# Kernel optimization log

Hardware: AMD Instinct MI355X
Metric: run time of the kernel (lower is better)

The kernel has to match this reference:

```python
import jax, jax.numpy as jnp
import numpy as np

E = 8        # n_experts
K = 2        # n_activated_experts (top_k)
D = 1024     # dim
B, N = 4, 4096
DC = 512     # dim_cond


def setup_inputs() -> dict:
    key = jax.random.key(0)
    ks = jax.random.split(key, 6)
    x = jax.random.normal(ks[0], (B, N, D), jnp.float32)
    cond = jax.random.normal(ks[1], (B, N, DC), jnp.float32)
    mask = jnp.ones((B, N), jnp.float32)
    W_shared = jax.random.normal(ks[2], (D, D), jnp.float32) * 0.02
    W_expert = jax.random.normal(ks[3], (D, D), jnp.float32) * 0.02
    W_gate = jax.random.normal(ks[4], (D, E - 1), jnp.float32) * 0.02
    bias = jnp.zeros((D,), jnp.float32)
    return dict(x=x, cond=cond, mask=mask, W_shared=W_shared,
                W_expert=W_expert, W_gate=W_gate, bias=bias)


def reference(x, cond, mask, W_shared, W_expert, W_gate, bias):
    b, n, d = x.shape
    T = b * n
    xf = x.reshape(T, d)

    # ---- router: softmax gate over E-1 logits, top-k, normalize ----
    scores = jax.nn.softmax(xf @ W_gate, axis=-1)            # [T, E-1]
    expert_weights, _ = jax.lax.top_k(scores, K)             # [T, K]
    expert_weights = expert_weights / expert_weights.sum(-1, keepdims=True)
    # uniform_expert_assignment=True: indices are arange % E
    expert_indices = (jnp.arange(T * K) % E).reshape(T, K)

    te = expert_indices.reshape(-1)                          # [T*K] flat assignments
    w = expert_weights.reshape(-1)                           # [T*K]

    capacity = (K * T) // E                                  # expert_capacity

    # ---- indices_and_bins: stable sort by expert, histogram, cumsum ----
    order = jnp.argsort(te, stable=True)                     # permutation into sorted order
    sorted_e = te[order]
    hist = jnp.bincount(te, length=E)                        # tokens_per_expert
    starts = jnp.concatenate([jnp.zeros((1,), hist.dtype), jnp.cumsum(hist)[:-1]])
    pos = jnp.arange(T * K) - starts[sorted_e]               # rank within expert bin
    valid = pos < capacity                                   # capacity drop
    dest = jnp.where(valid, sorted_e * capacity + pos, E * capacity)
    tok = order // K                                         # source token index

    # ---- binned_gather: [E*capacity, d] buffer, overflow row dropped ----
    gathered = jnp.zeros((E * capacity + 1, d), x.dtype).at[dest].set(xf[tok])
    gathered = gathered[:-1]

    # ---- expert compute on binned tokens ----
    y = gathered @ W_expert.T                                # [E*capacity, d]

    # ---- binned_scatter: weighted combine back to tokens ----
    contrib = w[order][:, None] * y[jnp.minimum(dest, E * capacity - 1)]
    moe_out = jnp.zeros((T, d), x.dtype).at[tok].add(
        jnp.where(valid[:, None], contrib, 0.0))

    shared = xf @ W_shared.T                                 # shared expert
    out = (shared + moe_out + bias).reshape(b, n, d)
    return out
```

## Files before the change

### kernel.cpp

```cpp
#include <hip/hip_runtime.h>
#include <hip/hip_bf16.h>
#include <stdint.h>

static constexpr int Mdim = 16384;
static constexpr int Ndim = 1024;
static constexpr int Kdim = 1024;
static constexpr int BM = 128, BN = 128, BK = 64;

typedef __attribute__((ext_vector_type(8))) __bf16 bf16x8;
typedef __attribute__((ext_vector_type(4))) float f32x4;
typedef __attribute__((ext_vector_type(8))) unsigned short ushort8;

__device__ inline unsigned short f2bf_rn(float f) {
    union { float f; uint32_t u; } v; v.f = f;
    uint32_t u = v.u;
    uint32_t r = u + 0x7FFFu + ((u >> 16) & 1u);
    return (unsigned short)(r >> 16);
}

__device__ inline uint32_t pack_bf2(float a, float b) {
    union { float f; uint32_t u; } ua, ub;
    ua.f = a; ub.f = b;
    uint32_t x = ua.u + 0x8000u;
    uint32_t y = ub.u + 0x8000u;
    return (x >> 16) | (y & 0xFFFF0000u);
}

__global__ __launch_bounds__(256) void cvt_w_kernel(const float* __restrict__ ws,
                                                    const float* __restrict__ we,
                                                    unsigned short* __restrict__ wc) {
    const size_t i = ((size_t)blockIdx.x * 256 + threadIdx.x) * 8;
    const f32x4* p0 = (const f32x4*)(ws + i);
    const f32x4* p1 = (const f32x4*)(we + i);
    f32x4 a0 = p0[0], a1 = p0[1], b0 = p1[0], b1 = p1[1];
    ushort8 o;
    o[0] = f2bf_rn(a0[0] + b0[0]); o[1] = f2bf_rn(a0[1] + b0[1]);
    o[2] = f2bf_rn(a0[2] + b0[2]); o[3] = f2bf_rn(a0[3] + b0[3]);
    o[4] = f2bf_rn(a1[0] + b1[0]); o[5] = f2bf_rn(a1[1] + b1[1]);
    o[6] = f2bf_rn(a1[2] + b1[2]); o[7] = f2bf_rn(a1[3] + b1[3]);
    *(ushort8*)(wc + i) = o;
}

__device__ inline void gload16(const void* g, void* l) {
    __builtin_amdgcn_global_load_lds((const __attribute__((address_space(1))) void*)g,
                                     (__attribute__((address_space(3))) void*)l,
                                     16, 0, 0);
}

__global__ __launch_bounds__(256, 4) void gemm_fused(const float* __restrict__ X,
                                                     const unsigned short* __restrict__ Bt,
                                                     const float* __restrict__ bias,
                                                     float* __restrict__ C) {
    __shared__ unsigned short As[2 * BM * 32];
    __shared__ unsigned short Bs[2 * BN * 32];

    const int tid = threadIdx.x;
    const int wave = tid >> 6;
    const int lane = tid & 63;
    const int bid = blockIdx.x;
    const int bm = bid & 127;
    const int bn = bid >> 7;
    const int wm = (wave >> 1) * 64;
    const int wn = (wave & 1) * 64;

    const int cw0 = wave, cw1 = wave + 4;
    const int brow0 = cw0 * 16 + (lane >> 2);
    const int brow1 = cw1 * 16 + (lane >> 2);
    const int bcol = (lane & 3) * 8;
    const unsigned short* gB0 = Bt + (size_t)(bn * BN + brow0) * Kdim + bcol;
    const unsigned short* gB1 = Bt + (size_t)(bn * BN + brow1) * Kdim + bcol;
    unsigned short* lB0 = Bs + cw0 * 512 + lane * 8;
    unsigned short* lB1 = Bs + cw1 * 512 + lane * 8;

    const int arow = tid >> 3;
    const int acol4 = tid & 7;
    const float* gA = X + (size_t)(bm * BM + arow) * Kdim + acol4 * 4;
    unsigned short* lA = As + arow * 32 + acol4 * 4;

    const int fr = lane & 15;
    const int fq = lane >> 4;
    const int fk = fq * 8;

    f32x4 acc[4][4] = {};

    for (int kt = 0; kt < Kdim; kt += BK) {
        __syncthreads();
#pragma unroll
        for (int s = 0; s < 2; ++s) {
            gload16(gB0 + kt + s * 32, lB0 + s * 4096);
            gload16(gB1 + kt + s * 32, lB1 + s * 4096);
        }
        f32x4 av[2][4];
#pragma unroll
        for (int s = 0; s < 2; ++s)
#pragma unroll
            for (int u = 0; u < 4; ++u)
                av[s][u] = *(const f32x4*)(gA + (size_t)u * 32 * Kdim + kt + s * 32);
#pragma unroll
        for (int s = 0; s < 2; ++s)
#pragma unroll
            for (int u = 0; u < 4; ++u) {
                uint2 w;
                w.x = pack_bf2(av[s][u][0], av[s][u][1]);
                w.y = pack_bf2(av[s][u][2], av[s][u][3]);
                *(uint2*)(lA + s * 4096 + u * 1024) = w;
            }
        __syncthreads();

#pragma unroll
        for (int s = 0; s < 2; ++s) {
            bf16x8 af[4], bfr[4];
#pragma unroll
            for (int i = 0; i < 4; ++i)
                af[i] = *(const bf16x8*)(As + s * 4096 + (wm + i * 16 + fr) * 32 + fk);
#pragma unroll
            for (int j = 0; j < 4; ++j)
                bfr[j] = *(const bf16x8*)(Bs + s * 4096 + (wn + j * 16 + fr) * 32 + fk);
#pragma unroll
            for (int i = 0; i < 4; ++i)
#pragma unroll
                for (int j = 0; j < 4; ++j)
                    acc[i][j] = __builtin_amdgcn_mfma_f32_16x16x32_bf16(af[i], bfr[j], acc[i][j], 0, 0, 0);
        }
    }

#pragma unroll
    for (int j = 0; j < 4; ++j) {
        const int col = bn * BN + wn + j * 16 + fr;
        const float bv = bias[col];
#pragma unroll
        for (int i = 0; i < 4; ++i) {
            const int row = bm * BM + wm + i * 16 + fq * 4;
            float* p = C + (size_t)row * Ndim + col;
#pragma unroll
            for (int r = 0; r < 4; ++r)
                p[(size_t)r * Ndim] = acc[i][j][r] + bv;
        }
    }
}

extern "C" void kernel_launch(void* const* d_in, const int* in_sizes, int n_in,
                              void* d_out, int out_size, void* d_ws, size_t ws_size,
                              hipStream_t stream) {
    const float* x    = (const float*)d_in[0];
    const float* Wsh  = (const float*)d_in[3];
    const float* Wex  = (const float*)d_in[4];
    const float* bias = (const float*)d_in[6];
    float* out = (float*)d_out;

    unsigned short* Wbf = (unsigned short*)d_ws;

    hipLaunchKernelGGL(cvt_w_kernel, dim3((Ndim * Kdim) / (256 * 8)), dim3(256), 0, stream,
                       Wsh, Wex, Wbf);
    hipLaunchKernelGGL(gemm_fused, dim3((Mdim / BM) * (Ndim / BN)), dim3(256), 0, stream,
                       x, Wbf, bias, out);
}
```

Before: 185.7 us.

## Double-buffer LDS and prefetch A tiles two steps ahead in GEMM

Restructures the main GEMM loop into a software pipeline with double-buffered LDS tiles of K-depth 32. B tiles are loaded asynchronously into the next buffer, and fp32 A tiles are prefetched two steps ahead into registers, then converted and written one step ahead. This halves the barriers per K-step and aims to overlap global loads with MFMA work. In exchange it uses more registers, lowers the occupancy hint from 4 to 3 blocks, and relies on correct waits for the async LDS loads.

```diff
diff --git a/kernel.cpp b/kernel.cpp
--- a/kernel.cpp
+++ b/kernel.cpp
@@ -5,7 +5,8 @@
 static constexpr int Mdim = 16384;
 static constexpr int Ndim = 1024;
 static constexpr int Kdim = 1024;
-static constexpr int BM = 128, BN = 128, BK = 64;
+static constexpr int BM = 128, BN = 128, BK = 32;
+static constexpr int NT = Kdim / BK;
 
 typedef __attribute__((ext_vector_type(8))) __bf16 bf16x8;
 typedef __attribute__((ext_vector_type(4))) float f32x4;
@@ -47,12 +48,12 @@
                                      16, 0, 0);
 }
 
-__global__ __launch_bounds__(256, 4) void gemm_fused(const float* __restrict__ X,
-                                                     const unsigned short* __restrict__ Bt,
-                                                     const float* __restrict__ bias,
-                                                     float* __restrict__ C) {
-    __shared__ unsigned short As[2 * BM * 32];
-    __shared__ unsigned short Bs[2 * BN * 32];
+__global__ __launch_bounds__(256, 3) void gemm_pipe(const float* __restrict__ X,
+                                                    const unsigned short* __restrict__ Bt,
+                                                    const float* __restrict__ bias,
+                                                    float* __restrict__ C) {
+    __shared__ unsigned short As[2][BM * BK];
+    __shared__ unsigned short Bs[2][BN * BK];
 
     const int tid = threadIdx.x;
     const int wave = tid >> 6;
@@ -69,59 +70,62 @@
     const int bcol = (lane & 3) * 8;
     const unsigned short* gB0 = Bt + (size_t)(bn * BN + brow0) * Kdim + bcol;
     const unsigned short* gB1 = Bt + (size_t)(bn * BN + brow1) * Kdim + bcol;
-    unsigned short* lB0 = Bs + cw0 * 512 + lane * 8;
-    unsigned short* lB1 = Bs + cw1 * 512 + lane * 8;
 
     const int arow = tid >> 3;
     const int acol4 = tid & 7;
     const float* gA = X + (size_t)(bm * BM + arow) * Kdim + acol4 * 4;
-    unsigned short* lA = As + arow * 32 + acol4 * 4;
 
     const int fr = lane & 15;
     const int fq = lane >> 4;
     const int fk = fq * 8;
 
+    f32x4 av[2][4];
+
+    auto issueA = [&](int t, int s) {
+#pragma unroll
+        for (int u = 0; u < 4; ++u)
+            av[s][u] = *(const f32x4*)(gA + (size_t)u * 32 * Kdim + t * BK);
+    };
+    auto issueB = [&](int t, int buf) {
+        gload16(gB0 + t * BK, &Bs[buf][cw0 * 512 + lane * 8]);
+        gload16(gB1 + t * BK, &Bs[buf][cw1 * 512 + lane * 8]);
+    };
+    auto writeA = [&](int s, int buf) {
+#pragma unroll
+        for (int u = 0; u < 4; ++u) {
+            uint2 w;
+            w.x = pack_bf2(av[s][u][0], av[s][u][1]);
+            w.y = pack_bf2(av[s][u][2], av[s][u][3]);
+            *(uint2*)(&As[buf][(arow + u * 32) * BK + acol4 * 4]) = w;
+        }
+    };
+
     f32x4 acc[4][4] = {};
 
-    for (int kt = 0; kt < Kdim; kt += BK) {
+    issueB(0, 0);
+    issueA(0, 0);
+    issueA(1, 1);
+    writeA(0, 0);
+
+    for (int t = 0; t < NT; ++t) {
+        const int cur = t & 1, nxt = cur ^ 1;
         __syncthreads();
+        if (t + 1 < NT) issueB(t + 1, nxt);
+        if (t + 2 < NT) issueA(t + 2, t & 1);
+        if (t + 1 < NT) writeA((t + 1) & 1, nxt);
+
+        bf16x8 af[4], bfr[4];
 #pragma unroll
-        for (int s = 0; s < 2; ++s) {
-            gload16(gB0 + kt + s * 32, lB0 + s * 4096);
-            gload16(gB1 + kt + s * 32, lB1 + s * 4096);
-        }
-        f32x4 av[2][4];
+        for (int i = 0; i < 4; ++i)
+            af[i] = *(const bf16x8*)(&As[cur][(wm + i * 16 + fr) * BK + fk]);
 #pragma unroll
-        for (int s = 0; s < 2; ++s)
+        for (int j = 0; j < 4; ++j)
+            bfr[j] = *(const bf16x8*)(&Bs[cur][(wn + j * 16 + fr) * BK + fk]);
 #pragma unroll
-            for (int u = 0; u < 4; ++u)
-                av[s][u] = *(const f32x4*)(gA + (size_t)u * 32 * Kdim + kt + s * 32);
-#pragma unroll
-        for (int s = 0; s < 2; ++s)
-#pragma unroll
-            for (int u = 0; u < 4; ++u) {
-                uint2 w;
-                w.x = pack_bf2(av[s][u][0], av[s][u][1]);
-                w.y = pack_bf2(av[s][u][2], av[s][u][3]);
-                *(uint2*)(lA + s * 4096 + u * 1024) = w;
-            }
-        __syncthreads();
-
-#pragma unroll
-        for (int s = 0; s < 2; ++s) {
-            bf16x8 af[4], bfr[4];
-#pragma unroll
-            for (int i = 0; i < 4; ++i)
-                af[i] = *(const bf16x8*)(As + s * 4096 + (wm + i * 16 + fr) * 32 + fk);
+        for (int i = 0; i < 4; ++i)
 #pragma unroll
             for (int j = 0; j < 4; ++j)
-                bfr[j] = *(const bf16x8*)(Bs + s * 4096 + (wn + j * 16 + fr) * 32 + fk);
-#pragma unroll
-            for (int i = 0; i < 4; ++i)
-#pragma unroll
-                for (int j = 0; j < 4; ++j)
-                    acc[i][j] = __builtin_amdgcn_mfma_f32_16x16x32_bf16(af[i], bfr[j], acc[i][j], 0, 0, 0);
-        }
+                acc[i][j] = __builtin_amdgcn_mfma_f32_16x16x32_bf16(af[i], bfr[j], acc[i][j], 0, 0, 0);
     }
 
 #pragma unroll
@@ -152,6 +156,6 @@
 
     hipLaunchKernelGGL(cvt_w_kernel, dim3((Ndim * Kdim) / (256 * 8)), dim3(256), 0, stream,
                        Wsh, Wex, Wbf);
-    hipLaunchKernelGGL(gemm_fused, dim3((Mdim / BM) * (Ndim / BN)), dim3(256), 0, stream,
+    hipLaunchKernelGGL(gemm_pipe, dim3((Mdim / BM) * (Ndim / BN)), dim3(256), 0, stream,
                        x, Wbf, bias, out);
 }
```

Measured after the change: 272.9 us. +47.0%, slower.

## Load A fragments directly into registers, stream only B through LDS

Applied to the files above, without the earlier changes.

Instead of converting the fp32 activation tile to bf16 in shared memory, each wave loads its own MFMA A fragments directly from global memory and packs them to bf16 in registers, prefetching the next k-subtile. Only B is staged in LDS, now with a 128-wide K phase, halving the number of barrier pairs. This removes the A LDS writes and reads but duplicates A global loads across the two waves sharing rows, uses less coalesced per-lane loads and more registers (occupancy hint lowered to 3).

```diff
diff --git a/kernel.cpp b/kernel.cpp
--- a/kernel.cpp
+++ b/kernel.cpp
@@ -5,11 +5,15 @@
 static constexpr int Mdim = 16384;
 static constexpr int Ndim = 1024;
 static constexpr int Kdim = 1024;
-static constexpr int BM = 128, BN = 128, BK = 64;
+static constexpr int BM = 128, BN = 128;
+static constexpr int PK = 128;
+static constexpr int NPH = Kdim / PK;
+static constexpr int KS = PK / 32;
 
 typedef __attribute__((ext_vector_type(8))) __bf16 bf16x8;
 typedef __attribute__((ext_vector_type(4))) float f32x4;
 typedef __attribute__((ext_vector_type(8))) unsigned short ushort8;
+typedef __attribute__((ext_vector_type(4))) unsigned int uint4v;
 
 __device__ inline unsigned short f2bf_rn(float f) {
     union { float f; uint32_t u; } v; v.f = f;
@@ -18,12 +22,10 @@
     return (unsigned short)(r >> 16);
 }
 
-__device__ inline uint32_t pack_bf2(float a, float b) {
+__device__ inline unsigned int pkbf(float a, float b) {
     union { float f; uint32_t u; } ua, ub;
     ua.f = a; ub.f = b;
-    uint32_t x = ua.u + 0x8000u;
-    uint32_t y = ub.u + 0x8000u;
-    return (x >> 16) | (y & 0xFFFF0000u);
+    return __builtin_amdgcn_perm(ub.u + 0x8000u, ua.u + 0x8000u, 0x07060302u);
 }
 
 __global__ __launch_bounds__(256) void cvt_w_kernel(const float* __restrict__ ws,
@@ -47,12 +49,11 @@
                                      16, 0, 0);
 }
 
-__global__ __launch_bounds__(256, 4) void gemm_fused(const float* __restrict__ X,
-                                                     const unsigned short* __restrict__ Bt,
-                                                     const float* __restrict__ bias,
-                                                     float* __restrict__ C) {
-    __shared__ unsigned short As[2 * BM * 32];
-    __shared__ unsigned short Bs[2 * BN * 32];
+__global__ __launch_bounds__(256, 3) void gemm_bstream(const float* __restrict__ X,
+                                                       const unsigned short* __restrict__ Bt,
+                                                       const float* __restrict__ bias,
+                                                       float* __restrict__ C) {
+    __shared__ unsigned short Bs[KS][BN * 32];
 
     const int tid = threadIdx.x;
     const int wave = tid >> 6;
@@ -62,6 +63,8 @@
     const int bn = bid >> 7;
     const int wm = (wave >> 1) * 64;
     const int wn = (wave & 1) * 64;
+    const int fr = lane & 15;
+    const int fq = lane >> 4;
 
     const int cw0 = wave, cw1 = wave + 4;
     const int brow0 = cw0 * 16 + (lane >> 2);
@@ -69,53 +72,56 @@
     const int bcol = (lane & 3) * 8;
     const unsigned short* gB0 = Bt + (size_t)(bn * BN + brow0) * Kdim + bcol;
     const unsigned short* gB1 = Bt + (size_t)(bn * BN + brow1) * Kdim + bcol;
-    unsigned short* lB0 = Bs + cw0 * 512 + lane * 8;
-    unsigned short* lB1 = Bs + cw1 * 512 + lane * 8;
+    unsigned short* lB0 = &Bs[0][cw0 * 512 + lane * 8];
+    unsigned short* lB1 = &Bs[0][cw1 * 512 + lane * 8];
 
-    const int arow = tid >> 3;
-    const int acol4 = tid & 7;
-    const float* gA = X + (size_t)(bm * BM + arow) * Kdim + acol4 * 4;
-    unsigned short* lA = As + arow * 32 + acol4 * 4;
-
-    const int fr = lane & 15;
-    const int fq = lane >> 4;
-    const int fk = fq * 8;
+    const float* gA[4];
+#pragma unroll
+    for (int i = 0; i < 4; ++i)
+        gA[i] = X + (size_t)(bm * BM + wm + i * 16 + fr) * Kdim + fq * 8;
 
     f32x4 acc[4][4] = {};
+    f32x4 av[2][4][2];
 
-    for (int kt = 0; kt < Kdim; kt += BK) {
+    for (int p = 0; p < NPH; ++p) {
+#pragma unroll
+        for (int i = 0; i < 4; ++i) {
+            const float* src = gA[i] + p * PK;
+            av[0][i][0] = *(const f32x4*)(src);
+            av[0][i][1] = *(const f32x4*)(src + 4);
+        }
         __syncthreads();
 #pragma unroll
-        for (int s = 0; s < 2; ++s) {
-            gload16(gB0 + kt + s * 32, lB0 + s * 4096);
-            gload16(gB1 + kt + s * 32, lB1 + s * 4096);
+        for (int s = 0; s < KS; ++s) {
+            gload16(gB0 + p * PK + s * 32, lB0 + s * 4096);
+            gload16(gB1 + p * PK + s * 32, lB1 + s * 4096);
         }
-        f32x4 av[2][4];
-#pragma unroll
-        for (int s = 0; s < 2; ++s)
-#pragma unroll
-            for (int u = 0; u < 4; ++u)
-                av[s][u] = *(const f32x4*)(gA + (size_t)u * 32 * Kdim + kt + s * 32);
-#pragma unroll
-        for (int s = 0; s < 2; ++s)
-#pragma unroll
-            for (int u = 0; u < 4; ++u) {
-                uint2 w;
-                w.x = pack_bf2(av[s][u][0], av[s][u][1]);
-                w.y = pack_bf2(av[s][u][2], av[s][u][3]);
-                *(uint2*)(lA + s * 4096 + u * 1024) = w;
-            }
         __syncthreads();
 
 #pragma unroll
-        for (int s = 0; s < 2; ++s) {
+        for (int s = 0; s < KS; ++s) {
+            if (s + 1 < KS) {
+#pragma unroll
+                for (int i = 0; i < 4; ++i) {
+                    const float* src = gA[i] + p * PK + (s + 1) * 32;
+                    av[(s + 1) & 1][i][0] = *(const f32x4*)(src);
+                    av[(s + 1) & 1][i][1] = *(const f32x4*)(src + 4);
+                }
+            }
             bf16x8 af[4], bfr[4];
 #pragma unroll
-            for (int i = 0; i < 4; ++i)
-                af[i] = *(const bf16x8*)(As + s * 4096 + (wm + i * 16 + fr) * 32 + fk);
+            for (int i = 0; i < 4; ++i) {
+                uint4v c;
+                c.x = pkbf(av[s & 1][i][0][0], av[s & 1][i][0][1]);
+                c.y = pkbf(av[s & 1][i][0][2], av[s & 1][i][0][3]);
+                c.z = pkbf(av[s & 1][i][1][0], av[s & 1][i][1][1]);
+                c.w = pkbf(av[s & 1][i][1][2], av[s & 1][i][1][3]);
+                union { uint4v u; bf16x8 v; } cv; cv.u = c;
+                af[i] = cv.v;
+            }
 #pragma unroll
             for (int j = 0; j < 4; ++j)
-                bfr[j] = *(const bf16x8*)(Bs + s * 4096 + (wn + j * 16 + fr) * 32 + fk);
+                bfr[j] = *(const bf16x8*)&Bs[s][(wn + j * 16 + fr) * 32 + fq * 8];
 #pragma unroll
             for (int i = 0; i < 4; ++i)
 #pragma unroll
@@ -131,10 +137,10 @@
 #pragma unroll
         for (int i = 0; i < 4; ++i) {
             const int row = bm * BM + wm + i * 16 + fq * 4;
-            float* p = C + (size_t)row * Ndim + col;
+            float* pc = C + (size_t)row * Ndim + col;
 #pragma unroll
             for (int r = 0; r < 4; ++r)
-                p[(size_t)r * Ndim] = acc[i][j][r] + bv;
+                pc[(size_t)r * Ndim] = acc[i][j][r] + bv;
         }
     }
 }
@@ -152,6 +158,6 @@
 
     hipLaunchKernelGGL(cvt_w_kernel, dim3((Ndim * Kdim) / (256 * 8)), dim3(256), 0, stream,
                        Wsh, Wex, Wbf);
-    hipLaunchKernelGGL(gemm_fused, dim3((Mdim / BM) * (Ndim / BN)), dim3(256), 0, stream,
+    hipLaunchKernelGGL(gemm_bstream, dim3((Mdim / BM) * (Ndim / BN)), dim3(256), 0, stream,
                        x, Wbf, bias, out);
 }
```

New measurement: 314.5 us. 1.69x slower.
